# Performance work log

Hardware: AMD Instinct MI355X
Metric: run time of the kernel (lower is better)

Reference implementation:

```python
import jax, jax.numpy as jnp
import numpy as np

B, T, V, E, H = 512, 40, 50000, 300, 512


def setup_inputs() -> dict:
    key = jax.random.key(0)
    ks = jax.random.split(key, 8)
    ref_expr_inds = jax.random.randint(ks[0], (B, T), 0, V)
    emb = jax.random.normal(ks[1], (V, E), dtype=jnp.float32) * 0.1
    w = lambda k, s: jax.random.normal(k, s, dtype=jnp.float32) * 0.05
    return dict(
        ref_expr_inds=ref_expr_inds,
        emb=emb,
        w_ih_f=w(ks[2], (3 * H, E)), w_hh_f=w(ks[3], (3 * H, H)),
        b_ih_f=jnp.zeros((3 * H,), jnp.float32), b_hh_f=jnp.zeros((3 * H,), jnp.float32),
        w_ih_b=w(ks[4], (3 * H, E)), w_hh_b=w(ks[5], (3 * H, H)),
        b_ih_b=jnp.zeros((3 * H,), jnp.float32), b_hh_b=jnp.zeros((3 * H,), jnp.float32),
    )


def _gru_dir(x, w_ih, w_hh, b_ih, b_hh):
    """Single-direction GRU (PyTorch math, gate order r,z,n). x: [B,T,E] -> [B,T,H]."""
    gi = jnp.einsum('bte,ge->btg', x, w_ih) + b_ih  # [B,T,3H], precomputed input gates

    def step(h, gi_t):
        gh = h @ w_hh.T + b_hh  # [B,3H]
        ir, iz, inn = jnp.split(gi_t, 3, axis=-1)
        hr, hz, hn = jnp.split(gh, 3, axis=-1)
        r = jax.nn.sigmoid(ir + hr)
        z = jax.nn.sigmoid(iz + hz)
        n = jnp.tanh(inn + r * hn)
        h_new = (1.0 - z) * n + z * h
        return h_new, h_new

    h0 = jnp.zeros((x.shape[0], w_hh.shape[1]), x.dtype)
    _, ys = jax.lax.scan(step, h0, jnp.swapaxes(gi, 0, 1))  # ys: [T,B,H]
    return jnp.swapaxes(ys, 0, 1)


def reference(ref_expr_inds, emb, w_ih_f, w_hh_f, b_ih_f, b_hh_f,
              w_ih_b, w_hh_b, b_ih_b, b_hh_b):
    valid = ref_expr_inds != 0  # True = real token (torch uses y_mask = (inds==0), then pools over ~y_mask)
    x = emb[ref_expr_inds]  # [B,T,E] embedding lookup
    y_f = _gru_dir(x, w_ih_f, w_hh_f, b_ih_f, b_hh_f)
    y_b = _gru_dir(x[:, ::-1], w_ih_b, w_hh_b, b_ih_b, b_hh_b)[:, ::-1]
    y_word = jnp.concatenate([y_f, y_b], axis=-1)  # [B,T,2H]
    neg = jnp.finfo(y_word.dtype).min
    # masked max-pool over valid tokens, vectorized (replaces python per-sample loop)
    y = jnp.max(jnp.where(valid[:, :, None], y_word, neg), axis=1, keepdims=True)  # [B,1,2H]
    return y
```

## Files before the change

kernel.cpp:

```cpp
#include <hip/hip_runtime.h>

typedef unsigned short u16;
typedef unsigned int u32;
typedef unsigned long long u64;
typedef short s16x8 __attribute__((ext_vector_type(8)));
typedef float f32x4 __attribute__((ext_vector_type(4)));

#define T_SEQ 40
#define EMB 300
#define KPAD 320
#define NCOL 3072
#define HS 262144

__device__ __forceinline__ u16 f2bf(float x) {
  u32 u = __builtin_bit_cast(u32, x);
  u32 r = (u + 0x7fffu + ((u >> 16) & 1u)) >> 16;
  return (u16)r;
}
__device__ __forceinline__ float bf2f(u16 h) {
  return __builtin_bit_cast(float, ((u32)h) << 16);
}
__device__ __forceinline__ float sigm(float x) {
  return 1.0f / (1.0f + __expf(-x));
}
__device__ __forceinline__ void coh_st32(u32* p, u32 v) {
  __hip_atomic_store(p, v, __ATOMIC_RELAXED, __HIP_MEMORY_SCOPE_AGENT);
}
__device__ __forceinline__ u64 coh_ld64(const u64* p) {
  return __hip_atomic_load((u64*)p, __ATOMIC_RELAXED, __HIP_MEMORY_SCOPE_AGENT);
}

__global__ void k_init(const int* __restrict__ idxs, u32* __restrict__ hpk,
                       u64* __restrict__ mask, int* __restrict__ bar) {
  int i = blockIdx.x * 256 + threadIdx.x;
  if (i < 2 * HS) coh_st32(&hpk[i], 0u);
  if (i < 256) coh_st32((u32*)&bar[i], 0u);
  if (i < 512) {
    u64 b = 0;
    for (int t = 0; t < T_SEQ; ++t)
      if (idxs[i * T_SEQ + t] != 0) b |= (1ull << t);
    mask[i] = b;
  }
}

__global__ void k_prep_emb(const float* __restrict__ emb, u16* __restrict__ emb16) {
  for (int idx = blockIdx.x * 256 + threadIdx.x; idx < 50000 * 160; idx += 4096 * 256) {
    int row = idx / 160, c2 = idx - row * 160;
    int c0 = 2 * c2;
    float v0 = (c0 < EMB) ? emb[(size_t)row * EMB + c0] : 0.0f;
    float v1 = (c0 + 1 < EMB) ? emb[(size_t)row * EMB + c0 + 1] : 0.0f;
    ((u32*)emb16)[(size_t)row * 160 + c2] = (u32)f2bf(v0) | ((u32)f2bf(v1) << 16);
  }
}

__global__ void k_prep_wih(const float* __restrict__ wf, const float* __restrict__ wb,
                           u16* __restrict__ wih) {
  int n = blockIdx.x, e = threadIdx.x;
  int dir = (n >= 1536);
  int g = n - dir * 1536;
  const float* src = dir ? wb : wf;
  float v = (e < EMB) ? src[(size_t)g * EMB + e] : 0.0f;
  wih[(size_t)n * KPAD + e] = f2bf(v);
}

__global__ void k_prep_whh(const float* __restrict__ wf, const float* __restrict__ wb,
                           u16* __restrict__ hi, u16* __restrict__ lo) {
  int n = blockIdx.x, k = threadIdx.x;
  int dir = (n >= 1536);
  int g = n - dir * 1536;
  float v = (dir ? wb : wf)[(size_t)g * 512 + k];
  u16 h = f2bf(v);
  hi[(size_t)n * 512 + k] = h;
  lo[(size_t)n * 512 + k] = f2bf(v - bf2f(h));
}

__global__ void k_prep_bias(const float* __restrict__ bihf, const float* __restrict__ bihb,
                            const float* __restrict__ bhhf, const float* __restrict__ bhhb,
                            float* __restrict__ bias_ih, float* __restrict__ bias_hh) {
  int i = blockIdx.x * 1024 + threadIdx.x;
  if (i >= 3072) return;
  int dir = (i >= 1536);
  int g = i - dir * 1536;
  bias_ih[i] = dir ? bihb[g] : bihf[g];
  bias_hh[i] = dir ? bhhb[g] : bhhf[g];
}

__global__ __launch_bounds__(256) void k_gi_gemm(
    const int* __restrict__ idxs, const float* __restrict__ emb,
    const u16* __restrict__ emb16, int use_emb16,
    const u16* __restrict__ wih, const float* __restrict__ bias_ih,
    u16* __restrict__ gi) {
  __shared__ __align__(16) char smem[34816];
  u16(*As)[40] = (u16(*)[40])smem;
  u16(*Bs)[40] = (u16(*)[40])(smem + 10240);
  u16(*Cs)[136] = (u16(*)[136])smem;

  const int m0 = blockIdx.x * 128;
  const int n0 = blockIdx.y * 128;
  const int t = threadIdx.x;
  const int w = t >> 6, l = t & 63;
  const int wm = (w >> 1) * 64, wn = (w & 1) * 64;
  const int lr = l & 15, lg = l >> 4;

  f32x4 acc[4][4];
#pragma unroll
  for (int i = 0; i < 4; ++i)
#pragma unroll
    for (int j = 0; j < 4; ++j) acc[i][j] = (f32x4)0.0f;

  const int arow = t >> 1, aseg = t & 1;
  const int tok = idxs[m0 + arow];
  const float* aerow = emb + (size_t)tok * EMB;
  const u16* aerow16 = emb16 + (size_t)tok * KPAD;
  const u16* brow_p = wih + (size_t)(n0 + arow) * KPAD;

  for (int kc = 0; kc < 10; ++kc) {
    const int k0 = kc * 32;
    if (use_emb16) {
      *(uint4*)&As[arow][aseg * 16] = *(const uint4*)(aerow16 + k0 + aseg * 16);
      *(uint4*)(&As[arow][aseg * 16] + 8) = *(const uint4*)(aerow16 + k0 + aseg * 16 + 8);
    } else {
      int cb = k0 + aseg * 16;
      u16* d = &As[arow][aseg * 16];
      if (cb + 15 < EMB) {
        const float4* s = (const float4*)(aerow + cb);
        float4 v0 = s[0], v1 = s[1], v2 = s[2], v3 = s[3];
        uint4 w0, w1;
        w0.x = (u32)f2bf(v0.x) | ((u32)f2bf(v0.y) << 16);
        w0.y = (u32)f2bf(v0.z) | ((u32)f2bf(v0.w) << 16);
        w0.z = (u32)f2bf(v1.x) | ((u32)f2bf(v1.y) << 16);
        w0.w = (u32)f2bf(v1.z) | ((u32)f2bf(v1.w) << 16);
        w1.x = (u32)f2bf(v2.x) | ((u32)f2bf(v2.y) << 16);
        w1.y = (u32)f2bf(v2.z) | ((u32)f2bf(v2.w) << 16);
        w1.z = (u32)f2bf(v3.x) | ((u32)f2bf(v3.y) << 16);
        w1.w = (u32)f2bf(v3.z) | ((u32)f2bf(v3.w) << 16);
        *(uint4*)d = w0;
        *(uint4*)(d + 8) = w1;
      } else {
#pragma unroll
        for (int e = 0; e < 16; ++e) {
          int c = cb + e;
          d[e] = (c < EMB) ? f2bf(aerow[c]) : (u16)0;
        }
      }
    }
    {
      const u16* s = brow_p + k0 + aseg * 16;
      u16* d = &Bs[arow][aseg * 16];
      *(uint4*)d = *(const uint4*)s;
      *(uint4*)(d + 8) = *(const uint4*)(s + 8);
    }
    __syncthreads();
    s16x8 av[4], bv[4];
#pragma unroll
    for (int i = 0; i < 4; ++i) av[i] = *(const s16x8*)&As[wm + i * 16 + lr][lg * 8];
#pragma unroll
    for (int j = 0; j < 4; ++j) bv[j] = *(const s16x8*)&Bs[wn + j * 16 + lr][lg * 8];
#pragma unroll
    for (int i = 0; i < 4; ++i)
#pragma unroll
      for (int j = 0; j < 4; ++j)
        acc[i][j] = __builtin_amdgcn_mfma_f32_16x16x32_bf16(av[i], bv[j], acc[i][j], 0, 0, 0);
    __syncthreads();
  }

  float bj[4];
#pragma unroll
  for (int j = 0; j < 4; ++j) bj[j] = bias_ih[n0 + wn + j * 16 + lr];
#pragma unroll
  for (int i = 0; i < 4; ++i)
#pragma unroll
    for (int j = 0; j < 4; ++j)
#pragma unroll
      for (int r = 0; r < 4; ++r)
        Cs[wm + i * 16 + lg * 4 + r][wn + j * 16 + lr] = f2bf(acc[i][j][r] + bj[j]);
  __syncthreads();
#pragma unroll
  for (int rr = t >> 4; rr < 128; rr += 16) {
    const int cseg = (t & 15) * 8;
    *(uint4*)(gi + (size_t)(m0 + rr) * NCOL + n0 + cseg) = *(const uint4*)&Cs[rr][cseg];
  }
}

__global__ __launch_bounds__(512, 2) void k_gru_persist(
    const u16* __restrict__ whh_hi, const u16* __restrict__ whh_lo,
    const float* __restrict__ bias_hh, const u16* __restrict__ gi,
    const u64* __restrict__ mask, u32* __restrict__ hpk,
    float* __restrict__ ymax, int* __restrict__ bar) {
  extern __shared__ u16 wlds[];
  const int bid = blockIdx.x;
  const int G = bid & 7;
  const int jt = bid >> 3;
  const int mt = G >> 1, dir = G & 1;
  const int m0 = mt * 128, j0 = jt * 16;
  const int wbase = dir * 1536;
  const int t = threadIdx.x;
  const int w = t >> 6, l = t & 63, lr = l & 15, lg = l >> 4;

  for (int c = t; c < 3072; c += 512) {
    const int col = c % 48, kcg = c / 48;
    const int g = col >> 4, jj = col & 15;
    const int k = (kcg >> 2) * 32 + (kcg & 3) * 8;
    const size_t off = (size_t)(wbase + g * 512 + j0 + jj) * 512 + k;
    *(uint4*)&wlds[c * 8] = *(const uint4*)(whh_hi + off);
    *(uint4*)&wlds[24576 + c * 8] = *(const uint4*)(whh_lo + off);
  }
  const int j = j0 + lr;
  const float bR = bias_hh[wbase + j];
  const float bZ = bias_hh[wbase + 512 + j];
  const float bN = bias_hh[wbase + 1024 + j];
  u64 mk[4];
  float hprev[4], ym[4];
#pragma unroll
  for (int r = 0; r < 4; ++r) {
    mk[r] = mask[m0 + w * 16 + lg * 4 + r];
    hprev[r] = 0.0f;
    ym[r] = -3.402823466e38f;
  }
  __syncthreads();

  const size_t abase = (size_t)(m0 + w * 16 + lr) * 512 + lg * 8;
  for (int s = 0; s < T_SEQ; ++s) {
    const int p = s & 1;
    const u32* hs = hpk + (size_t)(p * 2 + dir) * HS;
    u32* hd = hpk + (size_t)((p ^ 1) * 2 + dir) * HS;
    const int tok = dir ? (T_SEQ - 1 - s) : s;

    u16 gr[4], gz[4], gn[4];
#pragma unroll
    for (int r = 0; r < 4; ++r) {
      const int m = m0 + w * 16 + lg * 4 + r;
      const size_t gb = ((size_t)m * T_SEQ + tok) * NCOL + wbase + j;
      gr[r] = gi[gb];
      gz[r] = gi[gb + 512];
      gn[r] = gi[gb + 1024];
    }

    f32x4 acc[3];
    acc[0] = acc[1] = acc[2] = (f32x4)0.0f;
#pragma unroll
    for (int kc = 0; kc < 16; ++kc) {
      const u64* ap = (const u64*)(hs + abase + kc * 32);
      u64 q0 = coh_ld64(ap), q1 = coh_ld64(ap + 1), q2 = coh_ld64(ap + 2), q3 = coh_ld64(ap + 3);
      u32 hw[8];
      *(u64*)&hw[0] = q0; *(u64*)&hw[2] = q1; *(u64*)&hw[4] = q2; *(u64*)&hw[6] = q3;
      u32 ahw[4], alw[4];
#pragma unroll
      for (int i = 0; i < 4; ++i) {
        ahw[i] = (hw[2 * i] & 0xFFFFu) | (hw[2 * i + 1] << 16);
        alw[i] = (hw[2 * i] >> 16) | (hw[2 * i + 1] & 0xFFFF0000u);
      }
      const s16x8 ah = __builtin_bit_cast(s16x8, *(uint4*)ahw);
      const s16x8 al = __builtin_bit_cast(s16x8, *(uint4*)alw);
      const int bbase = ((kc * 4 + lg) * 48 + lr) * 8;
#pragma unroll
      for (int g = 0; g < 3; ++g) {
        const s16x8 bh = *(const s16x8*)&wlds[bbase + g * 128];
        const s16x8 bl = *(const s16x8*)&wlds[24576 + bbase + g * 128];
        acc[g] = __builtin_amdgcn_mfma_f32_16x16x32_bf16(ah, bh, acc[g], 0, 0, 0);
        acc[g] = __builtin_amdgcn_mfma_f32_16x16x32_bf16(al, bh, acc[g], 0, 0, 0);
        acc[g] = __builtin_amdgcn_mfma_f32_16x16x32_bf16(ah, bl, acc[g], 0, 0, 0);
      }
    }

#pragma unroll
    for (int r = 0; r < 4; ++r) {
      const int m = m0 + w * 16 + lg * 4 + r;
      const float rg = sigm(bf2f(gr[r]) + acc[0][r] + bR);
      const float zg = sigm(bf2f(gz[r]) + acc[1][r] + bZ);
      const float ng = tanhf(bf2f(gn[r]) + rg * (acc[2][r] + bN));
      const float hn = (1.0f - zg) * ng + zg * hprev[r];
      hprev[r] = hn;
      const u16 hh = f2bf(hn);
      const u16 hl = f2bf(hn - bf2f(hh));
      coh_st32(&hd[(size_t)m * 512 + j], (u32)hh | ((u32)hl << 16));
      if ((mk[r] >> tok) & 1ull) ym[r] = fmaxf(ym[r], hn);
    }

    if (s < T_SEQ - 1) {
      __syncthreads();
      if (t == 0) {
        __hip_atomic_fetch_add(&bar[G * 32], 1, __ATOMIC_RELAXED, __HIP_MEMORY_SCOPE_AGENT);
        const int target = 32 * (s + 1);
        while (__hip_atomic_load(&bar[G * 32], __ATOMIC_RELAXED, __HIP_MEMORY_SCOPE_AGENT) <
               target)
          __builtin_amdgcn_s_sleep(2);
      }
      __syncthreads();
    }
  }

#pragma unroll
  for (int r = 0; r < 4; ++r) {
    const int m = m0 + w * 16 + lg * 4 + r;
    ymax[(size_t)m * 1024 + dir * 512 + j] = ym[r];
  }
}

extern "C" void kernel_launch(void* const* d_in, const int* in_sizes, int n_in,
                              void* d_out, int out_size, void* d_ws, size_t ws_size,
                              hipStream_t stream) {
  const int* idxs = (const int*)d_in[0];
  const float* emb = (const float*)d_in[1];
  const float* wihf = (const float*)d_in[2];
  const float* whhf = (const float*)d_in[3];
  const float* bihf = (const float*)d_in[4];
  const float* bhhf = (const float*)d_in[5];
  const float* wihb = (const float*)d_in[6];
  const float* whhb = (const float*)d_in[7];
  const float* bihb = (const float*)d_in[8];
  const float* bhhb = (const float*)d_in[9];
  float* ymax = (float*)d_out;

  char* ws = (char*)d_ws;
  u16* whh_hi = (u16*)(ws + 0);
  u16* whh_lo = (u16*)(ws + 3145728);
  u16* wih = (u16*)(ws + 6291456);
  float* bias_ih = (float*)(ws + 8257536);
  float* bias_hh = (float*)(ws + 8269824);
  u32* hpk = (u32*)(ws + 8282112);
  u64* mask = (u64*)(ws + 12476416);
  int* bar = (int*)(ws + 12480512);
  u16* gi = (u16*)(ws + 12481536);
  u16* emb16 = (u16*)(ws + 138310656);
  const int use_emb16 = (ws_size >= 170310656ull) ? 1 : 0;

  k_init<<<2048, 256, 0, stream>>>(idxs, hpk, mask, bar);
  if (use_emb16) k_prep_emb<<<4096, 256, 0, stream>>>(emb, emb16);
  k_prep_wih<<<3072, 320, 0, stream>>>(wihf, wihb, wih);
  k_prep_whh<<<3072, 512, 0, stream>>>(whhf, whhb, whh_hi, whh_lo);
  k_prep_bias<<<3, 1024, 0, stream>>>(bihf, bihb, bhhf, bhhb, bias_ih, bias_hh);
  k_gi_gemm<<<dim3(160, 24), 256, 0, stream>>>(idxs, emb, emb16, use_emb16, wih, bias_ih, gi);

  hipFuncSetAttribute((const void*)k_gru_persist,
                      hipFuncAttributeMaxDynamicSharedMemorySize, 98304);
  k_gru_persist<<<dim3(256), dim3(512), 98304, stream>>>(whh_hi, whh_lo, bias_hh, gi, mask,
                                                         hpk, ymax, bar);
}
```

Measured before the change: 765.0 us.

## Bind GRU groups to XCDs, use plain h loads, prefetch gates, 8-slot h ring

The persistent GRU kernel now claims its group from the hardware XCC id and a per-XCD atomic slot counter. Each barrier group then lives on one XCD, which lets the hidden-state exchange use ordinary 128-bit loads and stores instead of agent-scope atomic loads and stores. The hidden-state buffer becomes an 8-deep ring that is zeroed inside the kernel and aliases the bf16 embedding copy, so the 2 MB init pass in k_init is dropped. The next step's input gates are prefetched before the barrier, and the spin sleep is shortened. The correctness of the plain loads depends on the XCD-local L2 coherence assumption and on exactly 32 blocks landing per XCD, which risks a deadlock or stale reads if scheduling differs.

```diff
diff --git a/kernel.cpp b/kernel.cpp
--- a/kernel.cpp
+++ b/kernel.cpp
@@ -23,18 +23,11 @@
 __device__ __forceinline__ float sigm(float x) {
   return 1.0f / (1.0f + __expf(-x));
 }
-__device__ __forceinline__ void coh_st32(u32* p, u32 v) {
-  __hip_atomic_store(p, v, __ATOMIC_RELAXED, __HIP_MEMORY_SCOPE_AGENT);
-}
-__device__ __forceinline__ u64 coh_ld64(const u64* p) {
-  return __hip_atomic_load((u64*)p, __ATOMIC_RELAXED, __HIP_MEMORY_SCOPE_AGENT);
-}
-
-__global__ void k_init(const int* __restrict__ idxs, u32* __restrict__ hpk,
-                       u64* __restrict__ mask, int* __restrict__ bar) {
+
+__global__ void k_init(const int* __restrict__ idxs, u64* __restrict__ mask,
+                       int* __restrict__ bar) {
   int i = blockIdx.x * 256 + threadIdx.x;
-  if (i < 2 * HS) coh_st32(&hpk[i], 0u);
-  if (i < 256) coh_st32((u32*)&bar[i], 0u);
+  if (i < 264) __hip_atomic_store(&bar[i], 0, __ATOMIC_RELAXED, __HIP_MEMORY_SCOPE_AGENT);
   if (i < 512) {
     u64 b = 0;
     for (int t = 0; t < T_SEQ; ++t)
@@ -188,15 +181,29 @@
     const u64* __restrict__ mask, u32* __restrict__ hpk,
     float* __restrict__ ymax, int* __restrict__ bar) {
   extern __shared__ u16 wlds[];
-  const int bid = blockIdx.x;
-  const int G = bid & 7;
-  const int jt = bid >> 3;
+  __shared__ int s_claim[2];
+  const int t = threadIdx.x;
+  if (t == 0) {
+    int xcd;
+    asm volatile("s_getreg_b32 %0, hwreg(HW_REG_XCC_ID)" : "=s"(xcd));
+    xcd &= 7;
+    int slot =
+        __hip_atomic_fetch_add(&bar[256 + xcd], 1, __ATOMIC_RELAXED, __HIP_MEMORY_SCOPE_AGENT);
+    s_claim[0] = xcd;
+    s_claim[1] = slot;
+  }
+  __syncthreads();
+  const int G = s_claim[0];
+  const int jt = s_claim[1];
   const int mt = G >> 1, dir = G & 1;
   const int m0 = mt * 128, j0 = jt * 16;
   const int wbase = dir * 1536;
-  const int t = threadIdx.x;
   const int w = t >> 6, l = t & 63, lr = l & 15, lg = l >> 4;
 
+  {
+    u32* z = hpk + ((size_t)dir * 512 + m0 + jt * 4) * 512;
+    for (int i = t; i < 2048; i += 512) z[i] = 0u;
+  }
   for (int c = t; c < 3072; c += 512) {
     const int col = c % 48, kcg = c / 48;
     const int g = col >> 4, jj = col & 15;
@@ -211,39 +218,49 @@
   const float bN = bias_hh[wbase + 1024 + j];
   u64 mk[4];
   float hprev[4], ym[4];
+  int mrow[4];
 #pragma unroll
   for (int r = 0; r < 4; ++r) {
-    mk[r] = mask[m0 + w * 16 + lg * 4 + r];
+    mrow[r] = m0 + w * 16 + lg * 4 + r;
+    mk[r] = mask[mrow[r]];
     hprev[r] = 0.0f;
     ym[r] = -3.402823466e38f;
   }
   __syncthreads();
-
-  const size_t abase = (size_t)(m0 + w * 16 + lr) * 512 + lg * 8;
-  for (int s = 0; s < T_SEQ; ++s) {
-    const int p = s & 1;
-    const u32* hs = hpk + (size_t)(p * 2 + dir) * HS;
-    u32* hd = hpk + (size_t)((p ^ 1) * 2 + dir) * HS;
-    const int tok = dir ? (T_SEQ - 1 - s) : s;
-
-    u16 gr[4], gz[4], gn[4];
+  if (t == 0) {
+    __hip_atomic_fetch_add(&bar[G * 32], 1, __ATOMIC_RELAXED, __HIP_MEMORY_SCOPE_AGENT);
+    while (__hip_atomic_load(&bar[G * 32], __ATOMIC_RELAXED, __HIP_MEMORY_SCOPE_AGENT) < 32)
+      __builtin_amdgcn_s_sleep(1);
+  }
+  __syncthreads();
+
+  u16 gr[4], gz[4], gn[4];
+  {
+    const int tok0 = dir ? (T_SEQ - 1) : 0;
 #pragma unroll
     for (int r = 0; r < 4; ++r) {
-      const int m = m0 + w * 16 + lg * 4 + r;
-      const size_t gb = ((size_t)m * T_SEQ + tok) * NCOL + wbase + j;
+      const size_t gb = ((size_t)mrow[r] * T_SEQ + tok0) * NCOL + wbase + j;
       gr[r] = gi[gb];
       gz[r] = gi[gb + 512];
       gn[r] = gi[gb + 1024];
     }
+  }
+
+  const size_t abase = (size_t)(m0 + w * 16 + lr) * 512 + lg * 8;
+  for (int s = 0; s < T_SEQ; ++s) {
+    const u32* hs = hpk + (size_t)((s & 7) * 2 + dir) * HS;
+    u32* hd = hpk + (size_t)(((s + 1) & 7) * 2 + dir) * HS;
+    const int tok = dir ? (T_SEQ - 1 - s) : s;
 
     f32x4 acc[3];
     acc[0] = acc[1] = acc[2] = (f32x4)0.0f;
 #pragma unroll
     for (int kc = 0; kc < 16; ++kc) {
-      const u64* ap = (const u64*)(hs + abase + kc * 32);
-      u64 q0 = coh_ld64(ap), q1 = coh_ld64(ap + 1), q2 = coh_ld64(ap + 2), q3 = coh_ld64(ap + 3);
+      const uint4* ap = (const uint4*)(hs + abase + kc * 32);
+      uint4 q0 = ap[0], q1 = ap[1];
       u32 hw[8];
-      *(u64*)&hw[0] = q0; *(u64*)&hw[2] = q1; *(u64*)&hw[4] = q2; *(u64*)&hw[6] = q3;
+      *(uint4*)&hw[0] = q0;
+      *(uint4*)&hw[4] = q1;
       u32 ahw[4], alw[4];
 #pragma unroll
       for (int i = 0; i < 4; ++i) {
@@ -265,7 +282,6 @@
 
 #pragma unroll
     for (int r = 0; r < 4; ++r) {
-      const int m = m0 + w * 16 + lg * 4 + r;
       const float rg = sigm(bf2f(gr[r]) + acc[0][r] + bR);
       const float zg = sigm(bf2f(gz[r]) + acc[1][r] + bZ);
       const float ng = tanhf(bf2f(gn[r]) + rg * (acc[2][r] + bN));
@@ -273,28 +289,34 @@
       hprev[r] = hn;
       const u16 hh = f2bf(hn);
       const u16 hl = f2bf(hn - bf2f(hh));
-      coh_st32(&hd[(size_t)m * 512 + j], (u32)hh | ((u32)hl << 16));
+      hd[(size_t)mrow[r] * 512 + j] = (u32)hh | ((u32)hl << 16);
       if ((mk[r] >> tok) & 1ull) ym[r] = fmaxf(ym[r], hn);
     }
 
     if (s < T_SEQ - 1) {
+      const int tok1 = dir ? (T_SEQ - 2 - s) : (s + 1);
+#pragma unroll
+      for (int r = 0; r < 4; ++r) {
+        const size_t gb = ((size_t)mrow[r] * T_SEQ + tok1) * NCOL + wbase + j;
+        gr[r] = gi[gb];
+        gz[r] = gi[gb + 512];
+        gn[r] = gi[gb + 1024];
+      }
       __syncthreads();
       if (t == 0) {
         __hip_atomic_fetch_add(&bar[G * 32], 1, __ATOMIC_RELAXED, __HIP_MEMORY_SCOPE_AGENT);
-        const int target = 32 * (s + 1);
+        const int target = 32 * (s + 2);
         while (__hip_atomic_load(&bar[G * 32], __ATOMIC_RELAXED, __HIP_MEMORY_SCOPE_AGENT) <
                target)
-          __builtin_amdgcn_s_sleep(2);
+          __builtin_amdgcn_s_sleep(1);
       }
       __syncthreads();
     }
   }
 
 #pragma unroll
-  for (int r = 0; r < 4; ++r) {
-    const int m = m0 + w * 16 + lg * 4 + r;
-    ymax[(size_t)m * 1024 + dir * 512 + j] = ym[r];
-  }
+  for (int r = 0; r < 4; ++r)
+    ymax[(size_t)mrow[r] * 1024 + dir * 512 + j] = ym[r];
 }
 
 extern "C" void kernel_launch(void* const* d_in, const int* in_sizes, int n_in,
@@ -318,14 +340,14 @@
   u16* wih = (u16*)(ws + 6291456);
   float* bias_ih = (float*)(ws + 8257536);
   float* bias_hh = (float*)(ws + 8269824);
-  u32* hpk = (u32*)(ws + 8282112);
-  u64* mask = (u64*)(ws + 12476416);
-  int* bar = (int*)(ws + 12480512);
-  u16* gi = (u16*)(ws + 12481536);
-  u16* emb16 = (u16*)(ws + 138310656);
-  const int use_emb16 = (ws_size >= 170310656ull) ? 1 : 0;
-
-  k_init<<<2048, 256, 0, stream>>>(idxs, hpk, mask, bar);
+  u64* mask = (u64*)(ws + 8282112);
+  int* bar = (int*)(ws + 8286208);
+  u16* emb16 = (u16*)(ws + 8290304);
+  u32* hpk = (u32*)(ws + 8290304);
+  u16* gi = (u16*)(ws + 40290304);
+  const int use_emb16 = (ws_size >= 166119424ull) ? 1 : 0;
+
+  k_init<<<2, 256, 0, stream>>>(idxs, mask, bar);
   if (use_emb16) k_prep_emb<<<4096, 256, 0, stream>>>(emb, emb16);
   k_prep_wih<<<3072, 320, 0, stream>>>(wihf, wihb, wih);
   k_prep_whh<<<3072, 512, 0, stream>>>(whhf, whhb, whh_hi, whh_lo);
```

Measured after the change: 1.025 ms. 1.34x slower.
